# Kernel tuning notes

Hardware: AMD Instinct MI355X
Metric: run time of the kernel (lower is better)

Reference implementation:

```python
import jax, jax.numpy as jnp
import numpy as np

N_EMBD = 1024
HEAD_SIZE = 128


def setup_inputs() -> dict:
    key = jax.random.key(0)
    k_x, k_w, k_cov, k_b = jax.random.split(key, 4)
    x = jax.random.normal(k_x, (16384, 2, N_EMBD), dtype=jnp.float32)
    # values_proj: nn.Linear(n_embd, head_size, bias=False) -> weight [head_size, n_embd]
    W = jax.random.normal(k_w, (HEAD_SIZE, N_EMBD), dtype=jnp.float32) * (N_EMBD ** -0.5)
    cov = jax.random.normal(k_cov, (HEAD_SIZE, HEAD_SIZE), dtype=jnp.float32) * (HEAD_SIZE ** -0.5)
    bias = jax.random.normal(k_b, (HEAD_SIZE,), dtype=jnp.float32)
    return {"x": x, "W": W, "cov": cov, "bias": bias}


def reference(x, W, cov, bias):
    # x: [B, 2, E]; W: [H, E]; cov: [H, H]; bias: [H]
    values = jnp.einsum('be,he->bh', x[:, 0, :], W)  # [B, H]
    mask = jnp.einsum('be,he->bh', x[:, 1, :], W)    # [B, H]
    # diag_embed(mask) @ cov == mask[:, :, None] * cov  -> [B, H, H]
    coeffs = jax.nn.softmax(mask[:, :, None] * cov[None, :, :], axis=-1)
    # values.unsqueeze(1) @ coeffs + bias, then [:, 0, :]
    out = jnp.einsum('bh,bhk->bk', values, coeffs) + bias
    return out
```

## Files before the change

### kernel.cpp

```cpp
#include <hip/hip_runtime.h>

#define LOG2E 1.4426950408889634f

typedef __attribute__((ext_vector_type(8))) short frag_ab;
typedef __attribute__((ext_vector_type(4))) float frag_cd;

__device__ inline short f2bf(float f) {
    union { float f; unsigned u; } v; v.f = f;
    unsigned r = v.u + 0x7fffu + ((v.u >> 16) & 1u);
    return (short)(r >> 16);
}

template<int CTRL>
__device__ inline float dpp_ror_add(float x) {
    int t = __builtin_amdgcn_update_dpp(0, __builtin_bit_cast(int, x), CTRL, 0xf, 0xf, false);
    return x + __builtin_bit_cast(float, t);
}

#define GLD_TO_LDS(gp, lp)                                                              \
    __builtin_amdgcn_global_load_lds((const __attribute__((address_space(1))) void*)(gp), \
                                     (__attribute__((address_space(3))) void*)(lp), 16, 0, 0)

__global__ __launch_bounds__(256) void prep_kernel(const float* __restrict__ W,
                                                   short* __restrict__ wbf) {
    int g = blockIdx.x * 256 + threadIdx.x;
    int h = g >> 7;
    int k0 = (g & 127) << 3;
    const float* src = W + h * 1024 + k0;
    float4 w0 = *(const float4*)src;
    float4 w1 = *(const float4*)(src + 4);
    frag_ab af;
    af[0] = f2bf(w0.x); af[1] = f2bf(w0.y); af[2] = f2bf(w0.z); af[3] = f2bf(w0.w);
    af[4] = f2bf(w1.x); af[5] = f2bf(w1.y); af[6] = f2bf(w1.z); af[7] = f2bf(w1.w);
    int c = k0 >> 6, s = (k0 >> 5) & 1, kg = (k0 >> 3) & 3;
    int nt = h >> 4, m = h & 15, lane = kg * 16 + m;
    int dst = (((c * 8 + nt) * 2 + s) * 64 + lane) * 8;
    *(frag_ab*)(wbf + dst) = af;
}

__global__ __launch_bounds__(256, 2) void fused_kernel(const float* __restrict__ x,
                                                       const short* __restrict__ wbf,
                                                       const float* __restrict__ cov,
                                                       const float* __restrict__ bias,
                                                       float* __restrict__ out) {
    __shared__ __align__(16) char smem[64 * 132 * 4];
    __shared__ float obuf[4][16][132];

    const int tid = threadIdx.x;
    const int lane = tid & 63, wave = tid >> 6;
    const int m = lane & 15, kg = lane >> 4;
    const long rowbase = (long)blockIdx.x * 64 + wave * 16;
    const float* xrow = x + (rowbase + m) * 1024 + kg * 8;

    const float bias_own = bias[tid & 127];

    frag_cd acc[8];
#pragma unroll
    for (int nt = 0; nt < 8; ++nt) acc[nt] = (frag_cd){0.f, 0.f, 0.f, 0.f};

    {
        const char* wc = (const char*)wbf;
        char* bd = smem;
        GLD_TO_LDS(wc + tid * 16,         bd + tid * 16);
        GLD_TO_LDS(wc + 4096 + tid * 16,  bd + 4096 + tid * 16);
        GLD_TO_LDS(wc + 8192 + tid * 16,  bd + 8192 + tid * 16);
        GLD_TO_LDS(wc + 12288 + tid * 16, bd + 12288 + tid * 16);
    }
    float4 a0 = *(const float4*)(xrow);
    float4 a1 = *(const float4*)(xrow + 4);
    float4 a2 = *(const float4*)(xrow + 32);
    float4 a3 = *(const float4*)(xrow + 36);
    __syncthreads();

    int cb = 0;
    for (int c = 0; c < 16; ++c) {
        float4 n0, n1, n2, n3;
        if (c < 15) {
            const char* wc = (const char*)wbf + (c + 1) * 16384;
            char* bd = smem + (cb ^ 1) * 16384;
            GLD_TO_LDS(wc + tid * 16,         bd + tid * 16);
            GLD_TO_LDS(wc + 4096 + tid * 16,  bd + 4096 + tid * 16);
            GLD_TO_LDS(wc + 8192 + tid * 16,  bd + 8192 + tid * 16);
            GLD_TO_LDS(wc + 12288 + tid * 16, bd + 12288 + tid * 16);
            const float* xn = xrow + (c + 1) * 64;
            n0 = *(const float4*)(xn);
            n1 = *(const float4*)(xn + 4);
            n2 = *(const float4*)(xn + 32);
            n3 = *(const float4*)(xn + 36);
        }
        frag_ab af0, af1;
        af0[0] = f2bf(a0.x); af0[1] = f2bf(a0.y); af0[2] = f2bf(a0.z); af0[3] = f2bf(a0.w);
        af0[4] = f2bf(a1.x); af0[5] = f2bf(a1.y); af0[6] = f2bf(a1.z); af0[7] = f2bf(a1.w);
        af1[0] = f2bf(a2.x); af1[1] = f2bf(a2.y); af1[2] = f2bf(a2.z); af1[3] = f2bf(a2.w);
        af1[4] = f2bf(a3.x); af1[5] = f2bf(a3.y); af1[6] = f2bf(a3.z); af1[7] = f2bf(a3.w);

        const char* bs = smem + cb * 16384;
#pragma unroll
        for (int nt = 0; nt < 8; ++nt) {
            frag_ab bf0 = *(const frag_ab*)(bs + (nt * 2 + 0) * 1024 + lane * 16);
            acc[nt] = __builtin_amdgcn_mfma_f32_16x16x32_bf16(af0, bf0, acc[nt], 0, 0, 0);
            frag_ab bf1 = *(const frag_ab*)(bs + (nt * 2 + 1) * 1024 + lane * 16);
            acc[nt] = __builtin_amdgcn_mfma_f32_16x16x32_bf16(af1, bf1, acc[nt], 0, 0, 0);
        }
        if (c < 15) { a0 = n0; a1 = n1; a2 = n2; a3 = n3; }
        __syncthreads();
        cb ^= 1;
    }

    const int i = tid >> 4;
    const int j = tid & 15;
    float covreg[8][8];
#pragma unroll
    for (int hh = 0; hh < 8; ++hh) {
        const float* cr = cov + (long)(i * 8 + hh) * 128 + j * 8;
        float4 c0 = *(const float4*)cr;
        float4 c1 = *(const float4*)(cr + 4);
        covreg[hh][0] = LOG2E * c0.x; covreg[hh][1] = LOG2E * c0.y;
        covreg[hh][2] = LOG2E * c0.z; covreg[hh][3] = LOG2E * c0.w;
        covreg[hh][4] = LOG2E * c1.x; covreg[hh][5] = LOG2E * c1.y;
        covreg[hh][6] = LOG2E * c1.z; covreg[hh][7] = LOG2E * c1.w;
    }
#pragma unroll
    for (int hh = 0; hh < 8; ++hh)
        asm volatile("" : "+v"(covreg[hh][0]), "+v"(covreg[hh][1]), "+v"(covreg[hh][2]),
                          "+v"(covreg[hh][3]), "+v"(covreg[hh][4]), "+v"(covreg[hh][5]),
                          "+v"(covreg[hh][6]), "+v"(covreg[hh][7]));

    float* vmf = (float*)smem;
#pragma unroll
    for (int nt = 0; nt < 8; ++nt)
#pragma unroll
        for (int r = 0; r < 4; ++r)
            vmf[(wave * 16 + kg * 4 + r) * 132 + nt * 16 + m] = acc[nt][r];
    __syncthreads();

    const long outbase = (long)blockIdx.x * 32 * 128;
    for (int r4 = 0; r4 < 8; ++r4) {
#pragma unroll
        for (int sb = 0; sb < 4; ++sb) {
            const int bl = r4 * 4 + sb;
            const float* vrow = vmf + (2 * bl) * 132 + i * 8;
            const float* mrow = vmf + (2 * bl + 1) * 132 + i * 8;
            float4 v0  = *(const float4*)(vrow);
            float4 v1  = *(const float4*)(vrow + 4);
            float4 mk0 = *(const float4*)(mrow);
            float4 mk1 = *(const float4*)(mrow + 4);
            float vh[8] = {v0.x, v0.y, v0.z, v0.w, v1.x, v1.y, v1.z, v1.w};
            float mh[8] = {mk0.x, mk0.y, mk0.z, mk0.w, mk1.x, mk1.y, mk1.z, mk1.w};
            float op[8] = {0.f, 0.f, 0.f, 0.f, 0.f, 0.f, 0.f, 0.f};
#pragma unroll
            for (int hh = 0; hh < 8; ++hh) {
                float mv = mh[hh];
                float p[8];
#pragma unroll
                for (int kk = 0; kk < 8; ++kk)
                    p[kk] = __builtin_amdgcn_exp2f(mv * covreg[hh][kk]);
                float s0 = p[0] + p[1], s1 = p[2] + p[3];
                float s2 = p[4] + p[5], s3 = p[6] + p[7];
                float lsum = (s0 + s1) + (s2 + s3);
                lsum = dpp_ror_add<0x121>(lsum);
                lsum = dpp_ror_add<0x122>(lsum);
                lsum = dpp_ror_add<0x124>(lsum);
                lsum = dpp_ror_add<0x128>(lsum);
                float w = vh[hh] * __builtin_amdgcn_rcpf(lsum);
#pragma unroll
                for (int kk = 0; kk < 8; ++kk) op[kk] = fmaf(w, p[kk], op[kk]);
            }
            *(float4*)&obuf[sb][i][j * 8]     = make_float4(op[0], op[1], op[2], op[3]);
            *(float4*)&obuf[sb][i][j * 8 + 4] = make_float4(op[4], op[5], op[6], op[7]);
        }
        __syncthreads();
        {
            const int k  = tid & 127;
            const int s0 = tid >> 7;
            float o0 = bias_own, o1 = bias_own;
#pragma unroll
            for (int ii = 0; ii < 16; ++ii) {
                o0 += obuf[s0][ii][k];
                o1 += obuf[s0 + 2][ii][k];
            }
            out[outbase + (r4 * 4 + s0) * 128 + k]     = o0;
            out[outbase + (r4 * 4 + s0 + 2) * 128 + k] = o1;
        }
        __syncthreads();
    }
}

extern "C" void kernel_launch(void* const* d_in, const int* in_sizes, int n_in,
                              void* d_out, int out_size, void* d_ws, size_t ws_size,
                              hipStream_t stream) {
    const float* x    = (const float*)d_in[0];
    const float* W    = (const float*)d_in[1];
    const float* cov  = (const float*)d_in[2];
    const float* bias = (const float*)d_in[3];
    float* out = (float*)d_out;

    const int B = in_sizes[0] / (2 * 1024);

    short* wbf = (short*)d_ws;

    prep_kernel<<<64, 256, 0, stream>>>(W, wbf);
    fused_kernel<<<(2 * B) / 64, 256, 0, stream>>>(x, wbf, cov, bias, out);
}
```

Measured before the change: 256.7 us.

## Shrink LDS footprint by staging one wave's results at a time for occupancy 4

```diff
diff --git a/kernel.cpp b/kernel.cpp
--- a/kernel.cpp
+++ b/kernel.cpp
@@ -38,13 +38,12 @@
     *(frag_ab*)(wbf + dst) = af;
 }
 
-__global__ __launch_bounds__(256, 2) void fused_kernel(const float* __restrict__ x,
+__global__ __launch_bounds__(256, 4) void fused_kernel(const float* __restrict__ x,
                                                        const short* __restrict__ wbf,
                                                        const float* __restrict__ cov,
                                                        const float* __restrict__ bias,
                                                        float* __restrict__ out) {
-    __shared__ __align__(16) char smem[64 * 132 * 4];
-    __shared__ float obuf[4][16][132];
+    __shared__ __align__(16) char smem[32768];
 
     const int tid = threadIdx.x;
     const int lane = tid & 63, wave = tid >> 6;
@@ -126,63 +125,65 @@
                           "+v"(covreg[hh][3]), "+v"(covreg[hh][4]), "+v"(covreg[hh][5]),
                           "+v"(covreg[hh][6]), "+v"(covreg[hh][7]));
 
-    float* vmf = (float*)smem;
-#pragma unroll
-    for (int nt = 0; nt < 8; ++nt)
-#pragma unroll
-        for (int r = 0; r < 4; ++r)
-            vmf[(wave * 16 + kg * 4 + r) * 132 + nt * 16 + m] = acc[nt][r];
-    __syncthreads();
-
+    float* vmf  = (float*)smem;
+    float* obuf = vmf + 16 * 132;
     const long outbase = (long)blockIdx.x * 32 * 128;
-    for (int r4 = 0; r4 < 8; ++r4) {
-#pragma unroll
-        for (int sb = 0; sb < 4; ++sb) {
-            const int bl = r4 * 4 + sb;
-            const float* vrow = vmf + (2 * bl) * 132 + i * 8;
-            const float* mrow = vmf + (2 * bl + 1) * 132 + i * 8;
-            float4 v0  = *(const float4*)(vrow);
-            float4 v1  = *(const float4*)(vrow + 4);
-            float4 mk0 = *(const float4*)(mrow);
-            float4 mk1 = *(const float4*)(mrow + 4);
-            float vh[8] = {v0.x, v0.y, v0.z, v0.w, v1.x, v1.y, v1.z, v1.w};
-            float mh[8] = {mk0.x, mk0.y, mk0.z, mk0.w, mk1.x, mk1.y, mk1.z, mk1.w};
-            float op[8] = {0.f, 0.f, 0.f, 0.f, 0.f, 0.f, 0.f, 0.f};
-#pragma unroll
-            for (int hh = 0; hh < 8; ++hh) {
-                float mv = mh[hh];
-                float p[8];
-#pragma unroll
-                for (int kk = 0; kk < 8; ++kk)
-                    p[kk] = __builtin_amdgcn_exp2f(mv * covreg[hh][kk]);
-                float s0 = p[0] + p[1], s1 = p[2] + p[3];
-                float s2 = p[4] + p[5], s3 = p[6] + p[7];
-                float lsum = (s0 + s1) + (s2 + s3);
-                lsum = dpp_ror_add<0x121>(lsum);
-                lsum = dpp_ror_add<0x122>(lsum);
-                lsum = dpp_ror_add<0x124>(lsum);
-                lsum = dpp_ror_add<0x128>(lsum);
-                float w = vh[hh] * __builtin_amdgcn_rcpf(lsum);
-#pragma unroll
-                for (int kk = 0; kk < 8; ++kk) op[kk] = fmaf(w, p[kk], op[kk]);
+
+    for (int w = 0; w < 4; ++w) {
+        if (wave == w) {
+#pragma unroll
+            for (int nt = 0; nt < 8; ++nt)
+#pragma unroll
+                for (int r = 0; r < 4; ++r)
+                    vmf[(kg * 4 + r) * 132 + nt * 16 + m] = acc[nt][r];
+        }
+        __syncthreads();
+
+        for (int r2 = 0; r2 < 4; ++r2) {
+#pragma unroll
+            for (int sb = 0; sb < 2; ++sb) {
+                const int lb = r2 * 2 + sb;
+                const float* vrow = vmf + (2 * lb) * 132 + i * 8;
+                const float* mrow = vmf + (2 * lb + 1) * 132 + i * 8;
+                float4 v0  = *(const float4*)(vrow);
+                float4 v1  = *(const float4*)(vrow + 4);
+                float4 mk0 = *(const float4*)(mrow);
+                float4 mk1 = *(const float4*)(mrow + 4);
+                float vh[8] = {v0.x, v0.y, v0.z, v0.w, v1.x, v1.y, v1.z, v1.w};
+                float mh[8] = {mk0.x, mk0.y, mk0.z, mk0.w, mk1.x, mk1.y, mk1.z, mk1.w};
+                float op[8] = {0.f, 0.f, 0.f, 0.f, 0.f, 0.f, 0.f, 0.f};
+#pragma unroll
+                for (int hh = 0; hh < 8; ++hh) {
+                    float mv = mh[hh];
+                    float p[8];
+#pragma unroll
+                    for (int kk = 0; kk < 8; ++kk)
+                        p[kk] = __builtin_amdgcn_exp2f(mv * covreg[hh][kk]);
+                    float s0 = p[0] + p[1], s1 = p[2] + p[3];
+                    float s2 = p[4] + p[5], s3 = p[6] + p[7];
+                    float lsum = (s0 + s1) + (s2 + s3);
+                    lsum = dpp_ror_add<0x121>(lsum);
+                    lsum = dpp_ror_add<0x122>(lsum);
+                    lsum = dpp_ror_add<0x124>(lsum);
+                    lsum = dpp_ror_add<0x128>(lsum);
+                    float wgt = vh[hh] * __builtin_amdgcn_rcpf(lsum);
+#pragma unroll
+                    for (int kk = 0; kk < 8; ++kk) op[kk] = fmaf(wgt, p[kk], op[kk]);
+                }
+                *(float4*)(obuf + (sb * 16 + i) * 132 + j * 8)     = make_float4(op[0], op[1], op[2], op[3]);
+                *(float4*)(obuf + (sb * 16 + i) * 132 + j * 8 + 4) = make_float4(op[4], op[5], op[6], op[7]);
             }
-            *(float4*)&obuf[sb][i][j * 8]     = make_float4(op[0], op[1], op[2], op[3]);
-            *(float4*)&obuf[sb][i][j * 8 + 4] = make_float4(op[4], op[5], op[6], op[7]);
-        }
-        __syncthreads();
-        {
-            const int k  = tid & 127;
-            const int s0 = tid >> 7;
-            float o0 = bias_own, o1 = bias_own;
-#pragma unroll
-            for (int ii = 0; ii < 16; ++ii) {
-                o0 += obuf[s0][ii][k];
-                o1 += obuf[s0 + 2][ii][k];
+            __syncthreads();
+            {
+                const int k  = tid & 127;
+                const int s0 = tid >> 7;
+                float o = bias_own;
+#pragma unroll
+                for (int ii = 0; ii < 16; ++ii) o += obuf[(s0 * 16 + ii) * 132 + k];
+                out[outbase + (w * 8 + r2 * 2 + s0) * 128 + k] = o;
             }
-            out[outbase + (r4 * 4 + s0) * 128 + k]     = o0;
-            out[outbase + (r4 * 4 + s0 + 2) * 128 + k] = o1;
-        }
-        __syncthreads();
+            __syncthreads();
+        }
     }
 }
 
```

After: 276.8 us. +7.8%, slower.

## Split fused kernel into separate projection and softmax-combine kernels

Applied to the files above, without the earlier changes.

```diff
diff --git a/kernel.cpp b/kernel.cpp
--- a/kernel.cpp
+++ b/kernel.cpp
@@ -21,6 +21,10 @@
     __builtin_amdgcn_global_load_lds((const __attribute__((address_space(1))) void*)(gp), \
                                      (__attribute__((address_space(3))) void*)(lp), 16, 0, 0)
 
+#define PACK_AF(af, p0, p1)                                                   \
+    af[0] = f2bf(p0.x); af[1] = f2bf(p0.y); af[2] = f2bf(p0.z); af[3] = f2bf(p0.w); \
+    af[4] = f2bf(p1.x); af[5] = f2bf(p1.y); af[6] = f2bf(p1.z); af[7] = f2bf(p1.w);
+
 __global__ __launch_bounds__(256) void prep_kernel(const float* __restrict__ W,
                                                    short* __restrict__ wbf) {
     int g = blockIdx.x * 256 + threadIdx.x;
@@ -30,21 +34,17 @@
     float4 w0 = *(const float4*)src;
     float4 w1 = *(const float4*)(src + 4);
     frag_ab af;
-    af[0] = f2bf(w0.x); af[1] = f2bf(w0.y); af[2] = f2bf(w0.z); af[3] = f2bf(w0.w);
-    af[4] = f2bf(w1.x); af[5] = f2bf(w1.y); af[6] = f2bf(w1.z); af[7] = f2bf(w1.w);
+    PACK_AF(af, w0, w1);
     int c = k0 >> 6, s = (k0 >> 5) & 1, kg = (k0 >> 3) & 3;
     int nt = h >> 4, m = h & 15, lane = kg * 16 + m;
     int dst = (((c * 8 + nt) * 2 + s) * 64 + lane) * 8;
     *(frag_ab*)(wbf + dst) = af;
 }
 
-__global__ __launch_bounds__(256, 2) void fused_kernel(const float* __restrict__ x,
-                                                       const short* __restrict__ wbf,
-                                                       const float* __restrict__ cov,
-                                                       const float* __restrict__ bias,
-                                                       float* __restrict__ out) {
-    __shared__ __align__(16) char smem[64 * 132 * 4];
-    __shared__ float obuf[4][16][132];
+__global__ __launch_bounds__(256, 2) void proj_kernel(const float* __restrict__ x,
+                                                      const short* __restrict__ wbf,
+                                                      float* __restrict__ vm) {
+    __shared__ __align__(16) char smem[32768];
 
     const int tid = threadIdx.x;
     const int lane = tid & 63, wave = tid >> 6;
@@ -52,19 +52,16 @@
     const long rowbase = (long)blockIdx.x * 64 + wave * 16;
     const float* xrow = x + (rowbase + m) * 1024 + kg * 8;
 
-    const float bias_own = bias[tid & 127];
-
     frag_cd acc[8];
 #pragma unroll
     for (int nt = 0; nt < 8; ++nt) acc[nt] = (frag_cd){0.f, 0.f, 0.f, 0.f};
 
     {
         const char* wc = (const char*)wbf;
-        char* bd = smem;
-        GLD_TO_LDS(wc + tid * 16,         bd + tid * 16);
-        GLD_TO_LDS(wc + 4096 + tid * 16,  bd + 4096 + tid * 16);
-        GLD_TO_LDS(wc + 8192 + tid * 16,  bd + 8192 + tid * 16);
-        GLD_TO_LDS(wc + 12288 + tid * 16, bd + 12288 + tid * 16);
+        GLD_TO_LDS(wc + tid * 16,         smem + tid * 16);
+        GLD_TO_LDS(wc + 4096 + tid * 16,  smem + 4096 + tid * 16);
+        GLD_TO_LDS(wc + 8192 + tid * 16,  smem + 8192 + tid * 16);
+        GLD_TO_LDS(wc + 12288 + tid * 16, smem + 12288 + tid * 16);
     }
     float4 a0 = *(const float4*)(xrow);
     float4 a1 = *(const float4*)(xrow + 4);
@@ -89,10 +86,8 @@
             n3 = *(const float4*)(xn + 36);
         }
         frag_ab af0, af1;
-        af0[0] = f2bf(a0.x); af0[1] = f2bf(a0.y); af0[2] = f2bf(a0.z); af0[3] = f2bf(a0.w);
-        af0[4] = f2bf(a1.x); af0[5] = f2bf(a1.y); af0[6] = f2bf(a1.z); af0[7] = f2bf(a1.w);
-        af1[0] = f2bf(a2.x); af1[1] = f2bf(a2.y); af1[2] = f2bf(a2.z); af1[3] = f2bf(a2.w);
-        af1[4] = f2bf(a3.x); af1[5] = f2bf(a3.y); af1[6] = f2bf(a3.z); af1[7] = f2bf(a3.w);
+        PACK_AF(af0, a0, a1);
+        PACK_AF(af1, a2, a3);
 
         const char* bs = smem + cb * 16384;
 #pragma unroll
@@ -107,12 +102,30 @@
         cb ^= 1;
     }
 
-    const int i = tid >> 4;
-    const int j = tid & 15;
-    float covreg[8][8];
 #pragma unroll
-    for (int hh = 0; hh < 8; ++hh) {
-        const float* cr = cov + (long)(i * 8 + hh) * 128 + j * 8;
+    for (int nt = 0; nt < 8; ++nt)
+#pragma unroll
+        for (int r = 0; r < 4; ++r) {
+            long row = rowbase + kg * 4 + r;
+            vm[row * 128 + nt * 16 + m] = acc[nt][r];
+        }
+}
+
+__global__ __launch_bounds__(512, 4) void combine_kernel(const float* __restrict__ vm,
+                                                         const float* __restrict__ cov,
+                                                         const float* __restrict__ bias,
+                                                         float* __restrict__ out) {
+    __shared__ float obuf[4][32][132];
+
+    const int t = threadIdx.x;
+    const int i = t >> 4;
+    const int j = t & 15;
+    const float bias_own = bias[t & 127];
+
+    float covreg[4][8];
+#pragma unroll
+    for (int hh = 0; hh < 4; ++hh) {
+        const float* cr = cov + (long)(i * 4 + hh) * 128 + j * 8;
         float4 c0 = *(const float4*)cr;
         float4 c1 = *(const float4*)(cr + 4);
         covreg[hh][0] = LOG2E * c0.x; covreg[hh][1] = LOG2E * c0.y;
@@ -120,36 +133,19 @@
         covreg[hh][4] = LOG2E * c1.x; covreg[hh][5] = LOG2E * c1.y;
         covreg[hh][6] = LOG2E * c1.z; covreg[hh][7] = LOG2E * c1.w;
     }
-#pragma unroll
-    for (int hh = 0; hh < 8; ++hh)
-        asm volatile("" : "+v"(covreg[hh][0]), "+v"(covreg[hh][1]), "+v"(covreg[hh][2]),
-                          "+v"(covreg[hh][3]), "+v"(covreg[hh][4]), "+v"(covreg[hh][5]),
-                          "+v"(covreg[hh][6]), "+v"(covreg[hh][7]));
 
-    float* vmf = (float*)smem;
-#pragma unroll
-    for (int nt = 0; nt < 8; ++nt)
-#pragma unroll
-        for (int r = 0; r < 4; ++r)
-            vmf[(wave * 16 + kg * 4 + r) * 132 + nt * 16 + m] = acc[nt][r];
-    __syncthreads();
-
-    const long outbase = (long)blockIdx.x * 32 * 128;
-    for (int r4 = 0; r4 < 8; ++r4) {
+    const long b0 = (long)blockIdx.x * 8;
+    for (int rr = 0; rr < 2; ++rr) {
 #pragma unroll
         for (int sb = 0; sb < 4; ++sb) {
-            const int bl = r4 * 4 + sb;
-            const float* vrow = vmf + (2 * bl) * 132 + i * 8;
-            const float* mrow = vmf + (2 * bl + 1) * 132 + i * 8;
-            float4 v0  = *(const float4*)(vrow);
-            float4 v1  = *(const float4*)(vrow + 4);
-            float4 mk0 = *(const float4*)(mrow);
-            float4 mk1 = *(const float4*)(mrow + 4);
-            float vh[8] = {v0.x, v0.y, v0.z, v0.w, v1.x, v1.y, v1.z, v1.w};
-            float mh[8] = {mk0.x, mk0.y, mk0.z, mk0.w, mk1.x, mk1.y, mk1.z, mk1.w};
+            const long b = b0 + rr * 4 + sb;
+            float4 v4 = *(const float4*)(vm + (2 * b) * 128 + i * 4);
+            float4 m4 = *(const float4*)(vm + (2 * b + 1) * 128 + i * 4);
+            float vh[4] = {v4.x, v4.y, v4.z, v4.w};
+            float mh[4] = {m4.x, m4.y, m4.z, m4.w};
             float op[8] = {0.f, 0.f, 0.f, 0.f, 0.f, 0.f, 0.f, 0.f};
 #pragma unroll
-            for (int hh = 0; hh < 8; ++hh) {
+            for (int hh = 0; hh < 4; ++hh) {
                 float mv = mh[hh];
                 float p[8];
 #pragma unroll
@@ -171,16 +167,12 @@
         }
         __syncthreads();
         {
-            const int k  = tid & 127;
-            const int s0 = tid >> 7;
-            float o0 = bias_own, o1 = bias_own;
+            const int k  = t & 127;
+            const int sb = t >> 7;
+            float o = bias_own;
 #pragma unroll
-            for (int ii = 0; ii < 16; ++ii) {
-                o0 += obuf[s0][ii][k];
-                o1 += obuf[s0 + 2][ii][k];
-            }
-            out[outbase + (r4 * 4 + s0) * 128 + k]     = o0;
-            out[outbase + (r4 * 4 + s0 + 2) * 128 + k] = o1;
+            for (int ii = 0; ii < 32; ++ii) o += obuf[sb][ii][k];
+            out[(b0 + rr * 4 + sb) * 128 + k] = o;
         }
         __syncthreads();
     }
@@ -198,7 +190,9 @@
     const int B = in_sizes[0] / (2 * 1024);
 
     short* wbf = (short*)d_ws;
+    float* vm  = (float*)(wbf + 128 * 1024);
 
     prep_kernel<<<64, 256, 0, stream>>>(W, wbf);
-    fused_kernel<<<(2 * B) / 64, 256, 0, stream>>>(x, wbf, cov, bias, out);
+    proj_kernel<<<(2 * B) / 64, 256, 0, stream>>>(x, wbf, vm);
+    combine_kernel<<<B / 8, 512, 0, stream>>>(vm, cov, bias, out);
 }
```

After: 255.3 us. Within noise of the previous version (-0.5%).
